# Optimization experiments

Measured on AMD Instinct MI355X. Metric: run time of the kernel, lower is better.

## Reference

```python
import jax, jax.numpy as jnp
import numpy as np

D_MODEL, D_STATE, D_CONV, EXPAND = 1024, 16, 4, 2
D_INNER = EXPAND * D_MODEL
EPS = 1e-6


def setup_inputs() -> dict:
    key = jax.random.key(0)
    ks = jax.random.split(key, 8)
    B, T = 2, 1024
    s = lambda fan_in: 1.0 / np.sqrt(fan_in)
    x = jax.random.normal(ks[0], (B, T, D_MODEL), dtype=jnp.float32)
    norm_w = jnp.ones((D_MODEL,), jnp.float32)
    in_proj_w = jax.random.normal(ks[1], (D_MODEL, 2 * D_INNER), jnp.float32) * s(D_MODEL)
    conv_w = jax.random.normal(ks[2], (D_INNER, 1, D_CONV), jnp.float32) * s(D_CONV)
    dt_w = jax.random.normal(ks[3], (D_INNER, D_INNER), jnp.float32) * s(D_INNER)
    dt_b = jnp.zeros((D_INNER,), jnp.float32)
    # A_log init: log(arange(1..d_state)) repeated over d_inner rows
    A_log = jnp.log(jnp.broadcast_to(jnp.arange(1, D_STATE + 1, dtype=jnp.float32), (D_INNER, D_STATE)))
    B_w = jax.random.normal(ks[4], (D_INNER, D_STATE), jnp.float32) * s(D_INNER)
    C_w = jax.random.normal(ks[5], (D_INNER, D_STATE), jnp.float32) * s(D_INNER)
    D_skip = jnp.ones((D_INNER,), jnp.float32)
    out_proj_w = jax.random.normal(ks[6], (D_INNER, D_MODEL), jnp.float32) * s(D_INNER)
    return {"x": x, "norm_w": norm_w, "in_proj_w": in_proj_w, "conv_w": conv_w,
            "dt_w": dt_w, "dt_b": dt_b, "A_log": A_log, "B_w": B_w, "C_w": C_w,
            "D_skip": D_skip, "out_proj_w": out_proj_w}


def _forward(x, norm_w, in_proj_w, conv_w, dt_w, dt_b, A_log, B_w, C_w, D_skip, out_proj_w):
    Bsz, T, _ = x.shape
    # RMSNorm
    xn = x * jax.lax.rsqrt(jnp.mean(x * x, axis=-1, keepdims=True) + EPS) * norm_w
    # in_proj + gated silu
    xg = xn @ in_proj_w                                  # [B,T,2*di]
    x_inner, gate = jnp.split(xg, 2, axis=-1)
    x_inner = x_inner * jax.nn.silu(gate)                # [B,T,di]
    # causal depthwise conv (torch pads both sides then takes first T == left-pad only)
    xc = jax.lax.conv_general_dilated(
        x_inner.transpose(0, 2, 1), conv_w, window_strides=(1,),
        padding=[(D_CONV - 1, 0)], feature_group_count=D_INNER,
        dimension_numbers=("NCH", "OIH", "NCH")).transpose(0, 2, 1)  # [B,T,di]
    dt = jax.nn.softplus(xc @ dt_w + dt_b)               # [B,T,di]
    A = -jnp.exp(A_log)                                  # [di,ds]
    Bm = xc @ B_w                                        # [B,T,ds]
    Cm = xc @ C_w                                        # [B,T,ds]
    A_bar = jnp.exp(dt[..., None] * A)                   # [B,T,di,ds]
    B_bar = dt[..., None] * Bm[:, :, None, :]            # [B,T,di,ds]

    def step(h, inp):
        a_t, b_t, xc_t, c_t = inp                        # [B,di,ds],[B,di,ds],[B,di],[B,ds]
        h = a_t * h + b_t * xc_t[..., None]
        y = jnp.einsum("bds,bs->bd", h, c_t) + D_skip * xc_t
        return h, y

    h0 = jnp.zeros((Bsz, D_INNER, D_STATE), x.dtype)
    xs = (A_bar.transpose(1, 0, 2, 3), B_bar.transpose(1, 0, 2, 3),
          xc.transpose(1, 0, 2), Cm.transpose(1, 0, 2))
    _, ys = jax.lax.scan(step, h0, xs)                   # ys: [T,B,di]
    out = ys.transpose(1, 0, 2) @ out_proj_w             # [B,T,d_model]
    return out


def reference(x, norm_w, in_proj_w, conv_w, dt_w, dt_b, A_log, B_w, C_w, D_skip, out_proj_w):
    return _forward(x, norm_w, in_proj_w, conv_w, dt_w, dt_b, A_log, B_w, C_w, D_skip, out_proj_w)
```

## Files before the change

kernel.cpp:

```cpp
#include <hip/hip_runtime.h>
#include <cmath>


#define SEQ    1024
#define BATCH  2
#define DMODEL 1024
#define DINNER 2048
#define DSTATE 16
#define NTOK   (BATCH * SEQ)
#define NCHUNK 32
#define CLEN   32
#define NEXT   2112

typedef __attribute__((ext_vector_type(8))) short short8;
typedef __attribute__((ext_vector_type(4))) float f32x4;

__device__ __forceinline__ unsigned short f2bf(float f) {
  unsigned int u = __float_as_uint(f);
  unsigned int r = (u + 0x7fffu + ((u >> 16) & 1u)) >> 16;
  return (unsigned short)r;
}
__device__ __forceinline__ float bf2f(unsigned short v) {
  return __uint_as_float((unsigned int)v << 16);
}
__device__ __forceinline__ float softplus_f(float x) {
  return (x > 20.f) ? x : log1pf(__expf(x));
}
__device__ __forceinline__ void gload_lds16(const void* g, void* l) {
  __builtin_amdgcn_global_load_lds(
      (const __attribute__((address_space(1))) unsigned int*)g,
      (__attribute__((address_space(3))) unsigned int*)l, 16, 0, 0);
}

template <int N>
__device__ __forceinline__ void wait_vmcnt() {
  if constexpr (N <= 0)      asm volatile("s_waitcnt vmcnt(0)" ::: "memory");
  else if constexpr (N == 1) asm volatile("s_waitcnt vmcnt(1)" ::: "memory");
  else if constexpr (N == 2) asm volatile("s_waitcnt vmcnt(2)" ::: "memory");
  else if constexpr (N == 3) asm volatile("s_waitcnt vmcnt(3)" ::: "memory");
  else if constexpr (N == 4) asm volatile("s_waitcnt vmcnt(4)" ::: "memory");
  else if constexpr (N == 5) asm volatile("s_waitcnt vmcnt(5)" ::: "memory");
  else if constexpr (N == 6) asm volatile("s_waitcnt vmcnt(6)" ::: "memory");
  else if constexpr (N == 8) asm volatile("s_waitcnt vmcnt(8)" ::: "memory");
  else                       asm volatile("s_waitcnt vmcnt(12)" ::: "memory");
}

__device__ __forceinline__ size_t tiled_off(int row, int k, int kblks) {
  return ((size_t)(row >> 4) * kblks + (k >> 5)) * 512
       + ((size_t)((row & 15) + (((k >> 3) & 3) << 4)) << 3) + (k & 7);
}

__global__ __launch_bounds__(256) void init_aneg_k(const float* __restrict__ A_log,
                                                   float* __restrict__ Aneg) {
  int i = blockIdx.x * 256 + threadIdx.x;
  Aneg[i] = -__expf(A_log[i]);
}

__global__ void transpose_cvt_k(const float* __restrict__ W, unsigned short* __restrict__ Wt,
                                int K, int N) {
  __shared__ float tile[32][33];
  int k0 = blockIdx.y * 32, n0 = blockIdx.x * 32;
  int tx = threadIdx.x, ty = threadIdx.y;
  int kblks = K >> 5;
#pragma unroll
  for (int i = 0; i < 32; i += 8)
    tile[ty + i][tx] = W[(size_t)(k0 + ty + i) * N + n0 + tx];
  __syncthreads();
#pragma unroll
  for (int i = 0; i < 32; i += 8)
    Wt[tiled_off(n0 + ty + i, k0 + tx, kblks)] = f2bf(tile[tx][ty + i]);
}

__global__ void build_w2t_k(const float* __restrict__ dt_w, const float* __restrict__ B_w,
                            const float* __restrict__ C_w, unsigned short* __restrict__ Wt) {
  __shared__ float tile[32][33];
  int k0 = blockIdx.x * 32, n0 = blockIdx.y * 32;
  int tx = threadIdx.x, ty = threadIdx.y;
  if (n0 < DINNER) {
#pragma unroll
    for (int i = 0; i < 32; i += 8)
      tile[ty + i][tx] = dt_w[(size_t)(k0 + ty + i) * DINNER + n0 + tx];
    __syncthreads();
#pragma unroll
    for (int i = 0; i < 32; i += 8)
      Wt[tiled_off(n0 + ty + i, k0 + tx, 64)] = f2bf(tile[tx][ty + i]);
  } else {
#pragma unroll
    for (int i = 0; i < 32; i += 8) {
      int n = n0 + ty + i;
      float v = 0.f;
      if (n < DINNER + 16) v = B_w[(size_t)(k0 + tx) * DSTATE + (n - DINNER)];
      else if (n < DINNER + 32) v = C_w[(size_t)(k0 + tx) * DSTATE + (n - DINNER - 16)];
      Wt[tiled_off(n, k0 + tx, 64)] = f2bf(v);
    }
  }
}

__global__ __launch_bounds__(256) void rmsnorm_k(const float* __restrict__ x,
                                                 const float* __restrict__ w,
                                                 unsigned short* __restrict__ xnbf) {
  int row = blockIdx.x, tid = threadIdx.x;
  const float4 v = *(const float4*)(x + (size_t)row * DMODEL + tid * 4);
  float ss = v.x * v.x + v.y * v.y + v.z * v.z + v.w * v.w;
#pragma unroll
  for (int off = 32; off > 0; off >>= 1) ss += __shfl_down(ss, off);
  __shared__ float red[4];
  if ((tid & 63) == 0) red[tid >> 6] = ss;
  __syncthreads();
  float tot = red[0] + red[1] + red[2] + red[3];
  float scale = rsqrtf(tot * (1.0f / DMODEL) + 1e-6f);
  const float4 wv = *(const float4*)(w + tid * 4);
  ushort4 o;
  o.x = f2bf(v.x * scale * wv.x);
  o.y = f2bf(v.y * scale * wv.y);
  o.z = f2bf(v.z * scale * wv.z);
  o.w = f2bf(v.w * scale * wv.w);
  *(ushort4*)(xnbf + tiled_off(row, tid * 4, DMODEL / 32)) = o;
}

template <int BM, int BN, int WM, int WN, int MODE, int SPLITZ>
__global__ __launch_bounds__(WM * WN * 64) void gemm_bf16_t(
    const unsigned short* __restrict__ At, const unsigned short* __restrict__ Btt,
    void* __restrict__ Cv, int M, int N, int K, int kstride, int ldc,
    const float* __restrict__ bias, float* __restrict__ Bm, float* __restrict__ Cm) {
  constexpr int NW = WM * WN;
  constexpr int WTM = BM / WM, WTN = BN / WN;
  constexpr int FM = WTM / 16, FN = WTN / 16;
  constexpr int ASUB = BM / 16, BSUB = BN / 16;
  constexpr int ALOAD = ASUB * 2, BLOAD = BSUB * 2;
  constexpr int LPW = (ALOAD + BLOAD) / NW;
  static_assert(ALOAD % NW == 0 && BLOAD % NW == 0, "uniform load split");
  __shared__ __align__(16) unsigned short Abuf[2][BM * 64];
  __shared__ __align__(16) unsigned short Bbuf[2][BN * 64];
  const int tid = threadIdx.x;
  const int wave = tid >> 6, lane = tid & 63;

  int lin = blockIdx.x + blockIdx.y * gridDim.x;
  int nwg = gridDim.x * gridDim.y;
  int swz = (lin & 7) * (nwg >> 3) + (lin >> 3);
  const int MT = gridDim.y;
  const int bm = (swz % MT) * BM, bn = (swz / MT) * BN;

  const int koff = SPLITZ ? blockIdx.z * (K >> 5) : 0;
  float* Cf = (float*)Cv;
  if (SPLITZ) Cf += (size_t)blockIdx.z * M * ldc;

  const int wm = wave / WN, wn = wave % WN;
  const unsigned short* Ag = At + ((size_t)(bm >> 4) * kstride + koff) * 512 + (lane << 3);
  const unsigned short* Bg = Btt + ((size_t)(bn >> 4) * kstride + koff) * 512 + (lane << 3);

  auto stage = [&](int buf, int t) {
#pragma unroll
    for (int i = wave; i < ALOAD; i += NW) {
      int s = i >> 1, kk = i & 1;
      gload_lds16(Ag + ((size_t)s * kstride + 2 * t + kk) * 512,
                  &Abuf[buf][(kk * ASUB + s) * 512]);
    }
#pragma unroll
    for (int i = wave; i < BLOAD; i += NW) {
      int s = i >> 1, kk = i & 1;
      gload_lds16(Bg + ((size_t)s * kstride + 2 * t + kk) * 512,
                  &Bbuf[buf][(kk * BSUB + s) * 512]);
    }
  };

  f32x4 acc[FM][FN] = {};
  const int nt = K / 64;
  stage(0, 0);
  stage(1, 1);
  for (int t = 0; t < nt; ++t) {
    const int cur = t & 1;
    if (t + 1 < nt) wait_vmcnt<LPW>();
    else            wait_vmcnt<0>();
    __builtin_amdgcn_s_barrier();
    short8 af[2][FM], bfr[2][FN];
#pragma unroll
    for (int kk = 0; kk < 2; ++kk) {
#pragma unroll
      for (int m = 0; m < FM; ++m)
        af[kk][m] = *(const short8*)&Abuf[cur][(kk * ASUB + wm * FM + m) * 512 + (lane << 3)];
#pragma unroll
      for (int n = 0; n < FN; ++n)
        bfr[kk][n] = *(const short8*)&Bbuf[cur][(kk * BSUB + wn * FN + n) * 512 + (lane << 3)];
    }
    asm volatile("s_waitcnt lgkmcnt(0)" ::: "memory");
    __builtin_amdgcn_sched_barrier(0);
    __builtin_amdgcn_s_barrier();
    if (t + 2 < nt) stage(cur, t + 2);
#pragma unroll
    for (int kk = 0; kk < 2; ++kk)
#pragma unroll
      for (int m = 0; m < FM; ++m)
#pragma unroll
        for (int n = 0; n < FN; ++n)
          acc[m][n] = __builtin_amdgcn_mfma_f32_16x16x32_bf16(af[kk][m], bfr[kk][n],
                                                              acc[m][n], 0, 0, 0);
  }

  const int rbase = bm + wm * WTM + (lane >> 4) * 4;
  const int cbase = bn + wn * WTN + (lane & 15);
#pragma unroll
  for (int m = 0; m < FM; ++m)
#pragma unroll
    for (int n = 0; n < FN; ++n) {
      int col = cbase + n * 16;
#pragma unroll
      for (int r = 0; r < 4; ++r) {
        int row = rbase + m * 16 + r;
        float v = acc[m][n][r];
        if (MODE == 0) {
          Cf[(size_t)row * ldc + col] = v;
        } else if (MODE == 1) {
          ((unsigned short*)Cv)[(size_t)row * ldc + col] = f2bf(v);
        } else {
          if (col < DINNER)
            ((float*)Cv)[(size_t)row * DINNER + col] = softplus_f(v + bias[col]);
          else if (col < DINNER + 16)
            Bm[(size_t)row * DSTATE + (col - DINNER)] = v;
          else if (col < DINNER + 32)
            Cm[(size_t)row * DSTATE + (col - DINNER - 16)] = v;
        }
      }
    }
}

__global__ __launch_bounds__(256) void reduce2_k(const float* __restrict__ P0,
                                                 const float* __restrict__ P1,
                                                 float* __restrict__ out) {
  int i = (blockIdx.x * 256 + threadIdx.x) * 4;
  float4 a = *(const float4*)(P0 + i);
  float4 b = *(const float4*)(P1 + i);
  float4 o = {a.x + b.x, a.y + b.y, a.z + b.z, a.w + b.w};
  *(float4*)(out + i) = o;
}

__global__ __launch_bounds__(256) void siluconv_k(const unsigned short* __restrict__ xg,
                                                  const float* __restrict__ w,
                                                  unsigned short* __restrict__ xcbf) {
  int idx = blockIdx.x * 256 + threadIdx.x;
  int d4 = (idx & 511) << 2;
  int tc = (idx >> 9) & 127;
  int b = idx >> 16;
  float4 w0 = *(const float4*)(w + (d4 + 0) * 4);
  float4 w1 = *(const float4*)(w + (d4 + 1) * 4);
  float4 w2 = *(const float4*)(w + (d4 + 2) * 4);
  float4 w3 = *(const float4*)(w + (d4 + 3) * 4);
  const float wj0[4] = {w0.x, w0.y, w0.z, w0.w};
  const float wj1[4] = {w1.x, w1.y, w1.z, w1.w};
  const float wj2[4] = {w2.x, w2.y, w2.z, w2.w};
  const float wj3[4] = {w3.x, w3.y, w3.z, w3.w};
  const unsigned short* pa = xg + (size_t)b * SEQ * (2 * DINNER) + d4;
  const unsigned short* pg = pa + DINNER;
  int t0 = tc * 8;
  float4 sA = {0.f, 0.f, 0.f, 0.f}, sB = sA, sC = sA;
  auto gated = [&](int t) {
    ushort4 av = *(const ushort4*)(pa + (size_t)t * (2 * DINNER));
    ushort4 gv = *(const ushort4*)(pg + (size_t)t * (2 * DINNER));
    float4 r;
    float gx = bf2f(gv.x), gy = bf2f(gv.y), gz = bf2f(gv.z), gw = bf2f(gv.w);
    r.x = bf2f(av.x) * (gx / (1.f + __expf(-gx)));
    r.y = bf2f(av.y) * (gy / (1.f + __expf(-gy)));
    r.z = bf2f(av.z) * (gz / (1.f + __expf(-gz)));
    r.w = bf2f(av.w) * (gw / (1.f + __expf(-gw)));
    return r;
  };
  if (t0 > 0) {
    sA = gated(t0 - 3);
    sB = gated(t0 - 2);
    sC = gated(t0 - 1);
  }
#pragma unroll
  for (int j = 0; j < 8; ++j) {
    int t = t0 + j;
    float4 sD = gated(t);
    float4 o;
    o.x = sA.x * wj0[0] + sB.x * wj0[1] + sC.x * wj0[2] + sD.x * wj0[3];
    o.y = sA.y * wj1[0] + sB.y * wj1[1] + sC.y * wj1[2] + sD.y * wj1[3];
    o.z = sA.z * wj2[0] + sB.z * wj2[1] + sC.z * wj2[2] + sD.z * wj2[3];
    o.w = sA.w * wj3[0] + sB.w * wj3[1] + sC.w * wj3[2] + sD.w * wj3[3];
    ushort4 ob = {f2bf(o.x), f2bf(o.y), f2bf(o.z), f2bf(o.w)};
    *(ushort4*)(xcbf + tiled_off(b * SEQ + t, d4, 64)) = ob;
    sA = sB; sB = sC; sC = sD;
  }
}

__global__ __launch_bounds__(256) void scan_local_k(const float* __restrict__ dt,
                                                    const unsigned short* __restrict__ xcbf,
                                                    const float* __restrict__ Bm,
                                                    const float* __restrict__ A,
                                                    float* __restrict__ hfin,
                                                    float* __restrict__ P) {
  int d = blockIdx.x * 256 + threadIdx.x;
  int c = blockIdx.y, b = blockIdx.z;
  float a[DSTATE], h[DSTATE];
#pragma unroll
  for (int s = 0; s < DSTATE; ++s) { a[s] = A[(size_t)d * DSTATE + s]; h[s] = 0.f; }
  float sdt = 0.f;
  int t0 = c * CLEN;
  for (int t = t0; t < t0 + CLEN; ++t) {
    size_t ro = (size_t)(b * SEQ + t);
    float dtv = dt[ro * DINNER + d];
    float xv = bf2f(xcbf[tiled_off((int)ro, d, 64)]);
    sdt += dtv;
    float bx = dtv * xv;
    float4 q0 = *(const float4*)(Bm + ro * DSTATE + 0);
    float4 q1 = *(const float4*)(Bm + ro * DSTATE + 4);
    float4 q2 = *(const float4*)(Bm + ro * DSTATE + 8);
    float4 q3 = *(const float4*)(Bm + ro * DSTATE + 12);
    float bm[DSTATE] = {q0.x, q0.y, q0.z, q0.w, q1.x, q1.y, q1.z, q1.w,
                        q2.x, q2.y, q2.z, q2.w, q3.x, q3.y, q3.z, q3.w};
#pragma unroll
    for (int s = 0; s < DSTATE; ++s) {
      float av = __expf(a[s] * dtv);
      h[s] = fmaf(av, h[s], bx * bm[s]);
    }
  }
  size_t o = ((size_t)(b * NCHUNK + c) * DINNER + d) * DSTATE;
#pragma unroll
  for (int s = 0; s < DSTATE; ++s) {
    hfin[o + s] = h[s];
    P[o + s] = __expf(a[s] * sdt);
  }
}

__global__ __launch_bounds__(256) void scan_chunks_k(float* hp, const float* __restrict__ P) {
  int j = blockIdx.x * 256 + threadIdx.x;
  int b = j / (DINNER * DSTATE);
  int r = j % (DINNER * DSTATE);
  float H = 0.f;
  for (int c = 0; c < NCHUNK; ++c) {
    size_t o = ((size_t)(b * NCHUNK + c) * DINNER * DSTATE) + r;
    float hf = hp[o];
    float pv = P[o];
    hp[o] = H;
    H = fmaf(pv, H, hf);
  }
}

__global__ __launch_bounds__(256) void scan_final_k(const float* __restrict__ dt,
                                                    const unsigned short* __restrict__ xcbf,
                                                    const float* __restrict__ Bm,
                                                    const float* __restrict__ Cm,
                                                    const float* __restrict__ A,
                                                    const float* __restrict__ Hprev,
                                                    const float* __restrict__ Dskip,
                                                    unsigned short* __restrict__ ysbf) {
  int d = blockIdx.x * 256 + threadIdx.x;
  int c = blockIdx.y, b = blockIdx.z;
  float a[DSTATE], h[DSTATE];
  size_t ho = ((size_t)(b * NCHUNK + c) * DINNER + d) * DSTATE;
#pragma unroll
  for (int s = 0; s < DSTATE; ++s) {
    a[s] = A[(size_t)d * DSTATE + s];
    h[s] = Hprev[ho + s];
  }
  float Dv = Dskip[d];
  int t0 = c * CLEN;
  for (int t = t0; t < t0 + CLEN; ++t) {
    size_t ro = (size_t)(b * SEQ + t);
    float dtv = dt[ro * DINNER + d];
    float xv = bf2f(xcbf[tiled_off((int)ro, d, 64)]);
    float bx = dtv * xv;
    float4 q0 = *(const float4*)(Bm + ro * DSTATE + 0);
    float4 q1 = *(const float4*)(Bm + ro * DSTATE + 4);
    float4 q2 = *(const float4*)(Bm + ro * DSTATE + 8);
    float4 q3 = *(const float4*)(Bm + ro * DSTATE + 12);
    float bm[DSTATE] = {q0.x, q0.y, q0.z, q0.w, q1.x, q1.y, q1.z, q1.w,
                        q2.x, q2.y, q2.z, q2.w, q3.x, q3.y, q3.z, q3.w};
    float4 r0 = *(const float4*)(Cm + ro * DSTATE + 0);
    float4 r1 = *(const float4*)(Cm + ro * DSTATE + 4);
    float4 r2 = *(const float4*)(Cm + ro * DSTATE + 8);
    float4 r3 = *(const float4*)(Cm + ro * DSTATE + 12);
    float cm[DSTATE] = {r0.x, r0.y, r0.z, r0.w, r1.x, r1.y, r1.z, r1.w,
                        r2.x, r2.y, r2.z, r2.w, r3.x, r3.y, r3.z, r3.w};
    float y = Dv * xv;
#pragma unroll
    for (int s = 0; s < DSTATE; ++s) {
      float av = __expf(a[s] * dtv);
      h[s] = fmaf(av, h[s], bx * bm[s]);
      y = fmaf(h[s], cm[s], y);
    }
    ysbf[tiled_off((int)ro, d, 64)] = f2bf(y);
  }
}

extern "C" void kernel_launch(void* const* d_in, const int* in_sizes, int n_in,
                              void* d_out, int out_size, void* d_ws, size_t ws_size,
                              hipStream_t stream) {
  (void)in_sizes; (void)n_in; (void)out_size; (void)ws_size;
  const float* x       = (const float*)d_in[0];
  const float* norm_w  = (const float*)d_in[1];
  const float* in_proj = (const float*)d_in[2];
  const float* conv_w  = (const float*)d_in[3];
  const float* dt_w    = (const float*)d_in[4];
  const float* dt_b    = (const float*)d_in[5];
  const float* A_log   = (const float*)d_in[6];
  const float* B_w     = (const float*)d_in[7];
  const float* C_w     = (const float*)d_in[8];
  const float* D_skip  = (const float*)d_in[9];
  const float* out_w   = (const float*)d_in[10];
  float* out = (float*)d_out;
  float* ws = (float*)d_ws;

  float* Aneg = ws;
  float* Bm   = ws + 32768;
  float* Cm   = ws + 65536;
  float* b0   = ws + 98304;
  unsigned short* xg = (unsigned short*)b0;
  float* dtb  = b0;
  float* hfin = b0 + 4194304;
  float* Pbuf = b0 + 6291456;
  float* outP = b0;
  unsigned short* xc_bf = (unsigned short*)(b0 + 8388608);
  unsigned short* ys_bf = (unsigned short*)(b0 + 10485760);
  float* Rw   = b0 + 12582912;
  unsigned short* in_wT  = (unsigned short*)Rw;
  unsigned short* W2t    = (unsigned short*)Rw;
  unsigned short* out_wT = (unsigned short*)Rw;
  unsigned short* xn_bf  = (unsigned short*)(b0 + 14745600);

  init_aneg_k<<<dim3(DINNER * DSTATE / 256), dim3(256), 0, stream>>>(A_log, Aneg);
  transpose_cvt_k<<<dim3(2 * DINNER / 32, DMODEL / 32), dim3(32, 8), 0, stream>>>(
      in_proj, in_wT, DMODEL, 2 * DINNER);
  rmsnorm_k<<<dim3(NTOK), dim3(256), 0, stream>>>(x, norm_w, xn_bf);
  gemm_bf16_t<128, 128, 2, 4, 1, 0>
      <<<dim3(2 * DINNER / 128, NTOK / 128), dim3(512), 0, stream>>>(
      xn_bf, in_wT, xg, NTOK, 2 * DINNER, DMODEL, DMODEL / 32, 2 * DINNER,
      nullptr, nullptr, nullptr);
  siluconv_k<<<dim3(NTOK * (DINNER / 4) / 8 / 256), dim3(256), 0, stream>>>(
      xg, conv_w, xc_bf);
  build_w2t_k<<<dim3(DINNER / 32, NEXT / 32), dim3(32, 8), 0, stream>>>(
      dt_w, B_w, C_w, W2t);
  gemm_bf16_t<128, 64, 4, 2, 2, 0>
      <<<dim3(NEXT / 64, NTOK / 128), dim3(512), 0, stream>>>(
      xc_bf, W2t, dtb, NTOK, NEXT, DINNER, DINNER / 32, DINNER, dt_b, Bm, Cm);
  scan_local_k<<<dim3(DINNER / 256, NCHUNK, BATCH), dim3(256), 0, stream>>>(
      dtb, xc_bf, Bm, Aneg, hfin, Pbuf);
  scan_chunks_k<<<dim3(BATCH * DINNER * DSTATE / 256), dim3(256), 0, stream>>>(
      hfin, Pbuf);
  scan_final_k<<<dim3(DINNER / 256, NCHUNK, BATCH), dim3(256), 0, stream>>>(
      dtb, xc_bf, Bm, Cm, Aneg, hfin, D_skip, ys_bf);
  transpose_cvt_k<<<dim3(DMODEL / 32, DINNER / 32), dim3(32, 8), 0, stream>>>(
      out_w, out_wT, DINNER, DMODEL);
  gemm_bf16_t<128, 64, 4, 2, 0, 1>
      <<<dim3(DMODEL / 64, NTOK / 128, 2), dim3(512), 0, stream>>>(
      ys_bf, out_wT, outP, NTOK, DMODEL, DINNER / 2, DINNER / 32, DMODEL,
      nullptr, nullptr, nullptr);
  reduce2_k<<<dim3(NTOK * DMODEL / 4 / 256), dim3(256), 0, stream>>>(
      outP, outP + (size_t)NTOK * DMODEL, out);
}
```

Before: 174.8 us.

## Restructure GEMM pipeline to triple-buffered 32-wide K steps with 4 waves

The bf16 GEMM now stages K in 32-wide slices into a three-deep LDS ring instead of 64-wide slices into a double buffer. This lets it issue the next prefetch right after one barrier and drop the second barrier and lgkmcnt wait per iteration. MFMA sections are wrapped in s_setprio, and all three GEMM launches go from 8 waves to 4 waves per block, so each wave covers a larger output tile. The aim is to cut synchronisation overhead and overlap loads with MFMA better, at the cost of twice as many loop iterations, more accumulator registers per wave, and fewer waves to hide latency.

```diff
diff --git a/kernel.cpp b/kernel.cpp
--- a/kernel.cpp
+++ b/kernel.cpp
@@ -35,14 +35,10 @@
 template <int N>
 __device__ __forceinline__ void wait_vmcnt() {
   if constexpr (N <= 0)      asm volatile("s_waitcnt vmcnt(0)" ::: "memory");
-  else if constexpr (N == 1) asm volatile("s_waitcnt vmcnt(1)" ::: "memory");
-  else if constexpr (N == 2) asm volatile("s_waitcnt vmcnt(2)" ::: "memory");
   else if constexpr (N == 3) asm volatile("s_waitcnt vmcnt(3)" ::: "memory");
   else if constexpr (N == 4) asm volatile("s_waitcnt vmcnt(4)" ::: "memory");
-  else if constexpr (N == 5) asm volatile("s_waitcnt vmcnt(5)" ::: "memory");
   else if constexpr (N == 6) asm volatile("s_waitcnt vmcnt(6)" ::: "memory");
-  else if constexpr (N == 8) asm volatile("s_waitcnt vmcnt(8)" ::: "memory");
-  else                       asm volatile("s_waitcnt vmcnt(12)" ::: "memory");
+  else                       asm volatile("s_waitcnt vmcnt(8)" ::: "memory");
 }
 
 __device__ __forceinline__ size_t tiled_off(int row, int k, int kblks) {
@@ -127,11 +123,10 @@
   constexpr int WTM = BM / WM, WTN = BN / WN;
   constexpr int FM = WTM / 16, FN = WTN / 16;
   constexpr int ASUB = BM / 16, BSUB = BN / 16;
-  constexpr int ALOAD = ASUB * 2, BLOAD = BSUB * 2;
-  constexpr int LPW = (ALOAD + BLOAD) / NW;
-  static_assert(ALOAD % NW == 0 && BLOAD % NW == 0, "uniform load split");
-  __shared__ __align__(16) unsigned short Abuf[2][BM * 64];
-  __shared__ __align__(16) unsigned short Bbuf[2][BN * 64];
+  constexpr int LPW = (ASUB + BSUB) / NW;
+  static_assert(ASUB % NW == 0 && BSUB % NW == 0, "uniform load split");
+  __shared__ __align__(16) unsigned short Abuf[3][BM * 32];
+  __shared__ __align__(16) unsigned short Bbuf[3][BN * 32];
   const int tid = threadIdx.x;
   const int wave = tid >> 6, lane = tid & 63;
 
@@ -151,50 +146,40 @@
 
   auto stage = [&](int buf, int t) {
 #pragma unroll
-    for (int i = wave; i < ALOAD; i += NW) {
-      int s = i >> 1, kk = i & 1;
-      gload_lds16(Ag + ((size_t)s * kstride + 2 * t + kk) * 512,
-                  &Abuf[buf][(kk * ASUB + s) * 512]);
-    }
-#pragma unroll
-    for (int i = wave; i < BLOAD; i += NW) {
-      int s = i >> 1, kk = i & 1;
-      gload_lds16(Bg + ((size_t)s * kstride + 2 * t + kk) * 512,
-                  &Bbuf[buf][(kk * BSUB + s) * 512]);
-    }
+    for (int s = wave; s < ASUB; s += NW)
+      gload_lds16(Ag + ((size_t)s * kstride + t) * 512, &Abuf[buf][s * 512]);
+#pragma unroll
+    for (int s = wave; s < BSUB; s += NW)
+      gload_lds16(Bg + ((size_t)s * kstride + t) * 512, &Bbuf[buf][s * 512]);
   };
 
   f32x4 acc[FM][FN] = {};
-  const int nt = K / 64;
+  const int nt = K / 32;
   stage(0, 0);
   stage(1, 1);
+  int cur = 0;
   for (int t = 0; t < nt; ++t) {
-    const int cur = t & 1;
     if (t + 1 < nt) wait_vmcnt<LPW>();
     else            wait_vmcnt<0>();
     __builtin_amdgcn_s_barrier();
-    short8 af[2][FM], bfr[2][FN];
-#pragma unroll
-    for (int kk = 0; kk < 2; ++kk) {
-#pragma unroll
-      for (int m = 0; m < FM; ++m)
-        af[kk][m] = *(const short8*)&Abuf[cur][(kk * ASUB + wm * FM + m) * 512 + (lane << 3)];
+    __builtin_amdgcn_sched_barrier(0);
+    int nxt = cur + 2; if (nxt >= 3) nxt -= 3;
+    if (t + 2 < nt) stage(nxt, t + 2);
+    short8 af[FM], bfr[FN];
+#pragma unroll
+    for (int m = 0; m < FM; ++m)
+      af[m] = *(const short8*)&Abuf[cur][(wm * FM + m) * 512 + (lane << 3)];
+#pragma unroll
+    for (int n = 0; n < FN; ++n)
+      bfr[n] = *(const short8*)&Bbuf[cur][(wn * FN + n) * 512 + (lane << 3)];
+    __builtin_amdgcn_s_setprio(1);
+#pragma unroll
+    for (int m = 0; m < FM; ++m)
 #pragma unroll
       for (int n = 0; n < FN; ++n)
-        bfr[kk][n] = *(const short8*)&Bbuf[cur][(kk * BSUB + wn * FN + n) * 512 + (lane << 3)];
-    }
-    asm volatile("s_waitcnt lgkmcnt(0)" ::: "memory");
-    __builtin_amdgcn_sched_barrier(0);
-    __builtin_amdgcn_s_barrier();
-    if (t + 2 < nt) stage(cur, t + 2);
-#pragma unroll
-    for (int kk = 0; kk < 2; ++kk)
-#pragma unroll
-      for (int m = 0; m < FM; ++m)
-#pragma unroll
-        for (int n = 0; n < FN; ++n)
-          acc[m][n] = __builtin_amdgcn_mfma_f32_16x16x32_bf16(af[kk][m], bfr[kk][n],
-                                                              acc[m][n], 0, 0, 0);
+        acc[m][n] = __builtin_amdgcn_mfma_f32_16x16x32_bf16(af[m], bfr[n], acc[m][n], 0, 0, 0);
+    __builtin_amdgcn_s_setprio(0);
+    cur = cur + 1; if (cur >= 3) cur = 0;
   }
 
   const int rbase = bm + wm * WTM + (lane >> 4) * 4;
@@ -423,16 +408,16 @@
   transpose_cvt_k<<<dim3(2 * DINNER / 32, DMODEL / 32), dim3(32, 8), 0, stream>>>(
       in_proj, in_wT, DMODEL, 2 * DINNER);
   rmsnorm_k<<<dim3(NTOK), dim3(256), 0, stream>>>(x, norm_w, xn_bf);
-  gemm_bf16_t<128, 128, 2, 4, 1, 0>
-      <<<dim3(2 * DINNER / 128, NTOK / 128), dim3(512), 0, stream>>>(
+  gemm_bf16_t<128, 128, 2, 2, 1, 0>
+      <<<dim3(2 * DINNER / 128, NTOK / 128), dim3(256), 0, stream>>>(
       xn_bf, in_wT, xg, NTOK, 2 * DINNER, DMODEL, DMODEL / 32, 2 * DINNER,
       nullptr, nullptr, nullptr);
   siluconv_k<<<dim3(NTOK * (DINNER / 4) / 8 / 256), dim3(256), 0, stream>>>(
       xg, conv_w, xc_bf);
   build_w2t_k<<<dim3(DINNER / 32, NEXT / 32), dim3(32, 8), 0, stream>>>(
       dt_w, B_w, C_w, W2t);
-  gemm_bf16_t<128, 64, 4, 2, 2, 0>
-      <<<dim3(NEXT / 64, NTOK / 128), dim3(512), 0, stream>>>(
+  gemm_bf16_t<128, 64, 2, 2, 2, 0>
+      <<<dim3(NEXT / 64, NTOK / 128), dim3(256), 0, stream>>>(
       xc_bf, W2t, dtb, NTOK, NEXT, DINNER, DINNER / 32, DINNER, dt_b, Bm, Cm);
   scan_local_k<<<dim3(DINNER / 256, NCHUNK, BATCH), dim3(256), 0, stream>>>(
       dtb, xc_bf, Bm, Aneg, hfin, Pbuf);
@@ -442,8 +427,8 @@
       dtb, xc_bf, Bm, Cm, Aneg, hfin, D_skip, ys_bf);
   transpose_cvt_k<<<dim3(DMODEL / 32, DINNER / 32), dim3(32, 8), 0, stream>>>(
       out_w, out_wT, DINNER, DMODEL);
-  gemm_bf16_t<128, 64, 4, 2, 0, 1>
-      <<<dim3(DMODEL / 64, NTOK / 128, 2), dim3(512), 0, stream>>>(
+  gemm_bf16_t<128, 64, 2, 2, 0, 1>
+      <<<dim3(DMODEL / 64, NTOK / 128, 2), dim3(256), 0, stream>>>(
       ys_bf, out_wT, outP, NTOK, DMODEL, DINNER / 2, DINNER / 32, DMODEL,
       nullptr, nullptr, nullptr);
   reduce2_k<<<dim3(NTOK * DMODEL / 4 / 256), dim3(256), 0, stream>>>(
```

Result: slower. 204.1 us (+16.8%).

## Add triple-buffered 256x128 bf16 GEMM with interleaved prefetch for in_proj

Applied to the files above, without the earlier changes.

Adds a new in_proj GEMM kernel with 256x128 tiles, three LDS stages in dynamic shared memory (~144KB) and a swizzled block order. Global-to-LDS prefetches for tile t+2 are spread across four MFMA phases, and s_setprio raises priority during the MFMA bursts. The aim is better overlap of memory loads with compute and more data reuse per block than the old 128x128 double-buffered kernel. The new path is taken only when the large LDS attribute is accepted, with the old kernel kept as a fallback; the vmcnt helper is also trimmed.

```diff
diff --git a/kernel.cpp b/kernel.cpp
--- a/kernel.cpp
+++ b/kernel.cpp
@@ -35,11 +35,6 @@
 template <int N>
 __device__ __forceinline__ void wait_vmcnt() {
   if constexpr (N <= 0)      asm volatile("s_waitcnt vmcnt(0)" ::: "memory");
-  else if constexpr (N == 1) asm volatile("s_waitcnt vmcnt(1)" ::: "memory");
-  else if constexpr (N == 2) asm volatile("s_waitcnt vmcnt(2)" ::: "memory");
-  else if constexpr (N == 3) asm volatile("s_waitcnt vmcnt(3)" ::: "memory");
-  else if constexpr (N == 4) asm volatile("s_waitcnt vmcnt(4)" ::: "memory");
-  else if constexpr (N == 5) asm volatile("s_waitcnt vmcnt(5)" ::: "memory");
   else if constexpr (N == 6) asm volatile("s_waitcnt vmcnt(6)" ::: "memory");
   else if constexpr (N == 8) asm volatile("s_waitcnt vmcnt(8)" ::: "memory");
   else                       asm volatile("s_waitcnt vmcnt(12)" ::: "memory");
@@ -116,6 +111,109 @@
   o.z = f2bf(v.z * scale * wv.z);
   o.w = f2bf(v.w * scale * wv.w);
   *(ushort4*)(xnbf + tiled_off(row, tid * 4, DMODEL / 32)) = o;
+}
+
+template <int MODE>
+__global__ __launch_bounds__(512) void gemm8p(
+    const unsigned short* __restrict__ At, const unsigned short* __restrict__ Btt,
+    void* __restrict__ Cv, int M, int N, int K, int kstride, int ldc) {
+  constexpr int SLOT = (256 + 128) * 64;
+  extern __shared__ __align__(16) unsigned short smem[];
+  const int tid = threadIdx.x;
+  const int wave = tid >> 6, lane = tid & 63;
+
+  int lin = blockIdx.x + blockIdx.y * gridDim.x;
+  int nwg = gridDim.x * gridDim.y;
+  int swz = (lin & 7) * (nwg >> 3) + (lin >> 3);
+  const int MT = gridDim.y;
+  const int bm = (swz % MT) * 256, bn = (swz / MT) * 128;
+
+  const int wm = wave >> 2, wn = wave & 3;
+  const unsigned short* Ag = At + ((size_t)(bm >> 4) * kstride) * 512 + (lane << 3);
+  const unsigned short* Bg = Btt + ((size_t)(bn >> 4) * kstride) * 512 + (lane << 3);
+
+  auto stageA = [&](int slot, int t, int rb, int kk) {
+    gload_lds16(Ag + ((size_t)rb * kstride + 2 * t + kk) * 512,
+                smem + slot * SLOT + (kk * 16 + rb) * 512);
+  };
+  auto stageB = [&](int slot, int t, int rb, int kk) {
+    gload_lds16(Bg + ((size_t)rb * kstride + 2 * t + kk) * 512,
+                smem + slot * SLOT + 16384 + (kk * 8 + rb) * 512);
+  };
+  auto stage_all = [&](int slot, int t) {
+    stageA(slot, t, wave, 0);
+    stageA(slot, t, wave, 1);
+    stageA(slot, t, wave + 8, 0);
+    stageA(slot, t, wave + 8, 1);
+    stageB(slot, t, wave, 0);
+    stageB(slot, t, wave, 1);
+  };
+
+  f32x4 acc[8][2] = {};
+  const int nt = K / 64;
+  stage_all(0, 0);
+  stage_all(1, 1);
+  wait_vmcnt<6>();
+  __builtin_amdgcn_s_barrier();
+  for (int t = 0; t < nt; ++t) {
+    const int slot = t % 3;
+    const int pslot = (t + 2) % 3;
+    const bool pf = (t + 2) < nt;
+    const unsigned short* bufA = smem + slot * SLOT;
+    const unsigned short* bufB = bufA + 16384;
+    short8 bfr[2];
+#pragma unroll
+    for (int ph = 0; ph < 4; ++ph) {
+      const int kk = ph >> 1, mh = ph & 1;
+      short8 af[4];
+#pragma unroll
+      for (int m = 0; m < 4; ++m)
+        af[m] = *(const short8*)(bufA + (kk * 16 + wm * 8 + mh * 4 + m) * 512 + (lane << 3));
+      if (mh == 0) {
+#pragma unroll
+        for (int n = 0; n < 2; ++n)
+          bfr[n] = *(const short8*)(bufB + (kk * 8 + wn * 2 + n) * 512 + (lane << 3));
+      }
+      if (pf) {
+        if (ph == 0)      { stageA(pslot, t + 2, wave, 0); stageA(pslot, t + 2, wave, 1); }
+        else if (ph == 1) { stageA(pslot, t + 2, wave + 8, 0); stageA(pslot, t + 2, wave + 8, 1); }
+        else if (ph == 2) { stageB(pslot, t + 2, wave, 0); }
+        else              { stageB(pslot, t + 2, wave, 1); }
+      }
+      asm volatile("s_waitcnt lgkmcnt(0)" ::: "memory");
+      __builtin_amdgcn_sched_barrier(0);
+      __builtin_amdgcn_s_setprio(1);
+#pragma unroll
+      for (int m = 0; m < 4; ++m)
+#pragma unroll
+        for (int n = 0; n < 2; ++n)
+          acc[mh * 4 + m][n] =
+              __builtin_amdgcn_mfma_f32_16x16x32_bf16(af[m], bfr[n], acc[mh * 4 + m][n], 0, 0, 0);
+      __builtin_amdgcn_s_setprio(0);
+      if (ph == 3) {
+        if (pf)              wait_vmcnt<6>();
+        else if (t + 1 < nt) wait_vmcnt<0>();
+      }
+      __builtin_amdgcn_s_barrier();
+    }
+  }
+
+  const int rbase = bm + wm * 128 + (lane >> 4) * 4;
+  const int cbase = bn + wn * 32 + (lane & 15);
+#pragma unroll
+  for (int m = 0; m < 8; ++m)
+#pragma unroll
+    for (int n = 0; n < 2; ++n) {
+      int col = cbase + n * 16;
+#pragma unroll
+      for (int r = 0; r < 4; ++r) {
+        int row = rbase + m * 16 + r;
+        if (MODE == 1)
+          ((unsigned short*)Cv)[(size_t)row * ldc + col] = f2bf(acc[m][n][r]);
+        else
+          ((float*)Cv)[(size_t)row * ldc + col] = acc[m][n][r];
+      }
+    }
 }
 
 template <int BM, int BN, int WM, int WN, int MODE, int SPLITZ>
@@ -170,8 +268,13 @@
   stage(1, 1);
   for (int t = 0; t < nt; ++t) {
     const int cur = t & 1;
-    if (t + 1 < nt) wait_vmcnt<LPW>();
-    else            wait_vmcnt<0>();
+    if (t + 1 < nt) {
+      if constexpr (LPW == 4) asm volatile("s_waitcnt vmcnt(4)" ::: "memory");
+      else if constexpr (LPW == 6) asm volatile("s_waitcnt vmcnt(6)" ::: "memory");
+      else asm volatile("s_waitcnt vmcnt(3)" ::: "memory");
+    } else {
+      asm volatile("s_waitcnt vmcnt(0)" ::: "memory");
+    }
     __builtin_amdgcn_s_barrier();
     short8 af[2][FM], bfr[2][FN];
 #pragma unroll
@@ -419,14 +522,23 @@
   unsigned short* out_wT = (unsigned short*)Rw;
   unsigned short* xn_bf  = (unsigned short*)(b0 + 14745600);
 
+  constexpr int kLds8p = 3 * (256 + 128) * 64 * 2;
+  hipError_t lds_ok = hipFuncSetAttribute(
+      (const void*)&gemm8p<1>, hipFuncAttributeMaxDynamicSharedMemorySize, kLds8p);
+
   init_aneg_k<<<dim3(DINNER * DSTATE / 256), dim3(256), 0, stream>>>(A_log, Aneg);
   transpose_cvt_k<<<dim3(2 * DINNER / 32, DMODEL / 32), dim3(32, 8), 0, stream>>>(
       in_proj, in_wT, DMODEL, 2 * DINNER);
   rmsnorm_k<<<dim3(NTOK), dim3(256), 0, stream>>>(x, norm_w, xn_bf);
-  gemm_bf16_t<128, 128, 2, 4, 1, 0>
-      <<<dim3(2 * DINNER / 128, NTOK / 128), dim3(512), 0, stream>>>(
-      xn_bf, in_wT, xg, NTOK, 2 * DINNER, DMODEL, DMODEL / 32, 2 * DINNER,
-      nullptr, nullptr, nullptr);
+  if (lds_ok == hipSuccess) {
+    gemm8p<1><<<dim3(2 * DINNER / 128, NTOK / 256), dim3(512), kLds8p, stream>>>(
+        xn_bf, in_wT, xg, NTOK, 2 * DINNER, DMODEL, DMODEL / 32, 2 * DINNER);
+  } else {
+    gemm_bf16_t<128, 128, 2, 4, 1, 0>
+        <<<dim3(2 * DINNER / 128, NTOK / 128), dim3(512), 0, stream>>>(
+        xn_bf, in_wT, xg, NTOK, 2 * DINNER, DMODEL, DMODEL / 32, 2 * DINNER,
+        nullptr, nullptr, nullptr);
+  }
   siluconv_k<<<dim3(NTOK * (DINNER / 4) / 8 / 256), dim3(256), 0, stream>>>(
       xg, conv_w, xc_bf);
   build_w2t_k<<<dim3(DINNER / 32, NEXT / 32), dim3(32, 8), 0, stream>>>(
```

After: 177.0 us. No clear change (+1.3%).
